# Performance work log

Measured on AMD Instinct MI355X. Metric: run time of the kernel, lower is better.

## Reference

```python
import jax, jax.numpy as jnp
import numpy as np

NEG_BIG = -9.0e15

def setup_inputs() -> dict:
    key = jax.random.key(0)
    k1, k2, k3, k4 = jax.random.split(key, 4)
    N, F_in, F_out = 2048, 512, 64
    x = jax.random.normal(k1, (N, F_in), dtype=jnp.float32)
    adj = jax.random.randint(k2, (N, N), 0, 2, dtype=jnp.int32)
    # xavier_uniform with gain=1.414
    def xavier(k, shape, gain=1.414):
        fan_in, fan_out = shape[0], shape[1]
        bound = gain * np.sqrt(6.0 / (fan_in + fan_out))
        return jax.random.uniform(k, shape, jnp.float32, -bound, bound)
    W = xavier(k3, (F_in, F_out))
    a = xavier(k4, (F_out, 1))
    return {"x": x, "adj": adj, "W": W, "a": a}

def reference(x, adj, W, a):
    h = x @ W                                  # [N, F_out]
    # pairwise |h_i - h_j| projected by a: e[i,j] = relu(sum_f |h_i,f - h_j,f| * a_f)
    diff = jnp.abs(h[:, None, :] - h[None, :, :])   # [N, N, F_out]
    e = jax.nn.relu(jnp.einsum('ijf,fo->ij', diff, a))  # [N, N]
    scores = jnp.where(adj > 0, e, NEG_BIG)
    attention = jax.nn.softmax(scores, axis=1)
    out = attention @ h                        # [N, F_out]
    return jax.nn.relu(out)                    # concat=True path
```

## Files before the change

kernel.cpp:

```cpp
#include <hip/hip_runtime.h>

#define Nn 2048
#define FIN 512
#define FO 64
#define SHIFT 20.0f
#define NJT 2
#define JSEG 1024
#define CHK 256

typedef __attribute__((ext_vector_type(8))) short bf16x8;
typedef __attribute__((ext_vector_type(4))) float f32x4;

__device__ __forceinline__ unsigned rne_bf16(float x) {
    unsigned u = __float_as_uint(x);
    return (u + 0x7FFFu + ((u >> 16) & 1u)) >> 16;
}
__device__ __forceinline__ float bf16_f32(unsigned s) { return __uint_as_float(s << 16); }

__global__ __launch_bounds__(256) void gat_xw(const float* __restrict__ x,
                                              const float* __restrict__ W,
                                              float* __restrict__ h) {
    __shared__ float part[2][2][FO];
    const int wave = threadIdx.x >> 6;
    const int lane = threadIdx.x & 63;
    const int rs = wave >> 1;
    const int kh = wave & 1;
    int row = blockIdx.x * 2 + rs;
    row = __builtin_amdgcn_readfirstlane(row);
    const float* xr = x + (size_t)row * FIN + kh * (FIN / 2);
    const float* Wp = W + (size_t)kh * (FIN / 2) * FO;
    float acc = 0.f;
#pragma unroll 2
    for (int k = 0; k < FIN / 2; k += 8) {
        float4 xa = *(const float4*)(xr + k);
        float4 xb = *(const float4*)(xr + k + 4);
        acc = fmaf(xa.x, Wp[(k + 0) * FO + lane], acc);
        acc = fmaf(xa.y, Wp[(k + 1) * FO + lane], acc);
        acc = fmaf(xa.z, Wp[(k + 2) * FO + lane], acc);
        acc = fmaf(xa.w, Wp[(k + 3) * FO + lane], acc);
        acc = fmaf(xb.x, Wp[(k + 4) * FO + lane], acc);
        acc = fmaf(xb.y, Wp[(k + 5) * FO + lane], acc);
        acc = fmaf(xb.z, Wp[(k + 6) * FO + lane], acc);
        acc = fmaf(xb.w, Wp[(k + 7) * FO + lane], acc);
    }
    part[rs][kh][lane] = acc;
    __syncthreads();
    if (threadIdx.x < 128) {
        const int r2 = threadIdx.x >> 6;
        const int l2 = threadIdx.x & 63;
        h[((size_t)blockIdx.x * 2 + r2) * FO + l2] = part[r2][0][l2] + part[r2][1][l2];
    }
}

__global__ __launch_bounds__(256) void gat_tr(const float* __restrict__ h,
                                              unsigned short* __restrict__ hbT_hi,
                                              unsigned short* __restrict__ hbT_lo) {
    __shared__ float t_s[64 * 68];
    const int tid = threadIdx.x;
    const int j0 = blockIdx.x * 64;
    for (int g4 = tid; g4 < 1024; g4 += 256) {
        float4 v = *(const float4*)(h + (size_t)j0 * FO + (size_t)g4 * 4);
        *(float4*)&t_s[(g4 >> 4) * 68 + (g4 & 15) * 4] = v;
    }
    __syncthreads();
    const int f = tid >> 2, q = tid & 3;
    unsigned* dh = (unsigned*)&hbT_hi[(size_t)f * Nn + j0 + q * 16];
    unsigned* dl = (unsigned*)&hbT_lo[(size_t)f * Nn + j0 + q * 16];
#pragma unroll
    for (int u = 0; u < 8; u++) {
        float x0 = t_s[(q * 16 + 2 * u) * 68 + f];
        float x1 = t_s[(q * 16 + 2 * u + 1) * 68 + f];
        unsigned h0 = rne_bf16(x0), h1 = rne_bf16(x1);
        dh[u] = h0 | (h1 << 16);
        float r0 = x0 - bf16_f32(h0), r1 = x1 - bf16_f32(h1);
        dl[u] = rne_bf16(r0) | (rne_bf16(r1) << 16);
    }
}

__global__ __launch_bounds__(256) void gat_attn7(const float* __restrict__ h,
                                                 const int* __restrict__ adj,
                                                 const float* __restrict__ a,
                                                 const unsigned short* __restrict__ hbT_hi,
                                                 const unsigned short* __restrict__ hbT_lo,
                                                 float* __restrict__ opart,
                                                 float* __restrict__ lpart) {
    __shared__ float hj_s[CHK * 64];
    __shared__ unsigned short Ph_s[16 * 264];
    __shared__ unsigned short Pl_s[16 * 264];

    const int tid = threadIdx.x;
    const int it = blockIdx.x >> 1;
    const int jt = blockIdx.x & 1;
    const int ib = it * 16;
    const int jb = jt * JSEG;
    const int ig = __builtin_amdgcn_readfirstlane(tid >> 7);
    const int jg = tid & 127;
    const int lane = tid & 63;
    const int w = tid >> 6;
    const int m = lane & 15;
    const int g = lane >> 4;

    float ls[8] = {0.f, 0.f, 0.f, 0.f, 0.f, 0.f, 0.f, 0.f};
    f32x4 acc = {0.f, 0.f, 0.f, 0.f};

    for (int jc = 0; jc < JSEG; jc += CHK) {
        __syncthreads();
        const float* hsrc = h + (size_t)(jb + jc) * FO;
        for (int g4 = tid; g4 < 4096; g4 += 256) {
            const int j = g4 >> 4, c = g4 & 15;
            *(float4*)&hj_s[j * 64 + ((c ^ (j & 7)) << 2)] =
                *(const float4*)(hsrc + (size_t)g4 * 4);
        }
        __syncthreads();

        const int j0 = jg * 2, j1 = j0 + 1;
        int2 am[8];
        const int* adjp = adj + (size_t)(ib + ig * 8) * Nn + (jb + jc + j0);
#pragma unroll
        for (int ii = 0; ii < 8; ii++) am[ii] = *(const int2*)(adjp + (size_t)ii * Nn);

        float e[8][2];
#pragma unroll
        for (int ii = 0; ii < 8; ii++) e[ii][0] = e[ii][1] = 0.f;

#pragma unroll 2
        for (int fq = 0; fq < 16; fq++) {
            const int f = fq * 4;
            const float4 av = *(const float4*)(a + f);
            const float4 hj0 = *(const float4*)&hj_s[j0 * 64 + ((fq ^ (j0 & 7)) << 2)];
            const float4 hj1 = *(const float4*)&hj_s[j1 * 64 + ((fq ^ (j1 & 7)) << 2)];
#pragma unroll
            for (int ii = 0; ii < 8; ii++) {
                const float4 hi = *(const float4*)(h + (size_t)(ib + ig * 8 + ii) * FO + f);
                e[ii][0] = fmaf(fabsf(hi.x - hj0.x), av.x, e[ii][0]);
                e[ii][0] = fmaf(fabsf(hi.y - hj0.y), av.y, e[ii][0]);
                e[ii][0] = fmaf(fabsf(hi.z - hj0.z), av.z, e[ii][0]);
                e[ii][0] = fmaf(fabsf(hi.w - hj0.w), av.w, e[ii][0]);
                e[ii][1] = fmaf(fabsf(hi.x - hj1.x), av.x, e[ii][1]);
                e[ii][1] = fmaf(fabsf(hi.y - hj1.y), av.y, e[ii][1]);
                e[ii][1] = fmaf(fabsf(hi.z - hj1.z), av.z, e[ii][1]);
                e[ii][1] = fmaf(fabsf(hi.w - hj1.w), av.w, e[ii][1]);
            }
        }

#pragma unroll
        for (int ii = 0; ii < 8; ii++) {
            const float p0 = (am[ii].x > 0) ? __expf(fmaxf(e[ii][0], 0.f) - SHIFT) : 0.f;
            const float p1 = (am[ii].y > 0) ? __expf(fmaxf(e[ii][1], 0.f) - SHIFT) : 0.f;
            ls[ii] += p0 + p1;
            const unsigned h0 = rne_bf16(p0), h1 = rne_bf16(p1);
            const float r0 = p0 - bf16_f32(h0), r1 = p1 - bf16_f32(h1);
            ((unsigned*)Ph_s)[(ig * 8 + ii) * 132 + jg] = h0 | (h1 << 16);
            ((unsigned*)Pl_s)[(ig * 8 + ii) * 132 + jg] =
                rne_bf16(r0) | (rne_bf16(r1) << 16);
        }
        __syncthreads();

        const size_t bbase = (size_t)(w * 16 + m) * Nn + (jb + jc);
#pragma unroll
        for (int ks = 0; ks < 8; ks++) {
            const bf16x8 af = *(const bf16x8*)&Ph_s[m * 264 + ks * 32 + g * 8];
            const bf16x8 al = *(const bf16x8*)&Pl_s[m * 264 + ks * 32 + g * 8];
            const bf16x8 bh = *(const bf16x8*)&hbT_hi[bbase + ks * 32 + g * 8];
            const bf16x8 bl = *(const bf16x8*)&hbT_lo[bbase + ks * 32 + g * 8];
            acc = __builtin_amdgcn_mfma_f32_16x16x32_bf16(af, bh, acc, 0, 0, 0);
            acc = __builtin_amdgcn_mfma_f32_16x16x32_bf16(af, bl, acc, 0, 0, 0);
            acc = __builtin_amdgcn_mfma_f32_16x16x32_bf16(al, bh, acc, 0, 0, 0);
        }
    }

    __syncthreads();
    float* red = hj_s;
#pragma unroll
    for (int ii = 0; ii < 8; ii++) red[(ig * 8 + ii) * 132 + jg] = ls[ii];
    __syncthreads();
    if (tid < 16) {
        float l = 0.f;
        for (int c2 = 0; c2 < 128; c2++) l += red[tid * 132 + c2];
        lpart[(size_t)jt * Nn + ib + tid] = l;
    }
#pragma unroll
    for (int r = 0; r < 4; r++)
        opart[((size_t)jt * Nn + ib + g * 4 + r) * FO + w * 16 + m] = acc[r];
}

__global__ __launch_bounds__(256) void gat_merge(const float* __restrict__ opart,
                                                 const float* __restrict__ lpart,
                                                 float* __restrict__ out) {
    const int t = blockIdx.x * 256 + threadIdx.x;
    const int i = t >> 6;
    const float o = opart[t] + opart[(size_t)Nn * FO + t];
    const float l = lpart[i] + lpart[Nn + i];
    out[t] = fmaxf(o / l, 0.f);
}

extern "C" void kernel_launch(void* const* d_in, const int* in_sizes, int n_in,
                              void* d_out, int out_size, void* d_ws, size_t ws_size,
                              hipStream_t stream) {
    const float* x   = (const float*)d_in[0];
    const int*   adj = (const int*)d_in[1];
    const float* W   = (const float*)d_in[2];
    const float* a   = (const float*)d_in[3];
    float* out = (float*)d_out;

    float* h     = (float*)d_ws;
    float* opart = h + (size_t)Nn * FO;
    float* lpart = opart + (size_t)NJT * Nn * FO;
    unsigned short* hbT_hi = (unsigned short*)(lpart + (size_t)NJT * Nn);
    unsigned short* hbT_lo = hbT_hi + (size_t)FO * Nn;

    gat_xw<<<dim3(1024), dim3(256), 0, stream>>>(x, W, h);
    gat_tr<<<dim3(32), dim3(256), 0, stream>>>(h, hbT_hi, hbT_lo);
    gat_attn7<<<dim3(256), dim3(256), 0, stream>>>(h, adj, a, hbT_hi, hbT_lo, opart, lpart);
    gat_merge<<<dim3(512), dim3(256), 0, stream>>>(opart, lpart, out);
}
```

Measured before the change: 140.3 us.

## Split attention over more j-segments chosen by workspace size, halve chunk size

The attention kernel now takes a runtime number of j-segments (2, 4 or 8, picked from the available workspace), launching up to 1024 blocks instead of 256 to fill more compute units. Each thread handles one j column instead of two, and the chunk size drops to 128 so shared memory shrinks and launch bounds request 3 blocks per unit. The shared h tile uses padding instead of an XOR swizzle. The merge kernel loops over the segments, which adds partial-result traffic and merge work for the extra parallelism.

Result: slower. 149.4 us (+6.5%).

```diff
diff --git a/kernel.cpp b/kernel.cpp
--- a/kernel.cpp
+++ b/kernel.cpp
@@ -4,9 +4,7 @@
 #define FIN 512
 #define FO 64
 #define SHIFT 20.0f
-#define NJT 2
-#define JSEG 1024
-#define CHK 256
+#define CHK 128
 
 typedef __attribute__((ext_vector_type(8))) short bf16x8;
 typedef __attribute__((ext_vector_type(4))) float f32x4;
@@ -77,22 +75,25 @@
     }
 }
 
-__global__ __launch_bounds__(256) void gat_attn7(const float* __restrict__ h,
-                                                 const int* __restrict__ adj,
-                                                 const float* __restrict__ a,
-                                                 const unsigned short* __restrict__ hbT_hi,
-                                                 const unsigned short* __restrict__ hbT_lo,
-                                                 float* __restrict__ opart,
-                                                 float* __restrict__ lpart) {
-    __shared__ float hj_s[CHK * 64];
-    __shared__ unsigned short Ph_s[16 * 264];
-    __shared__ unsigned short Pl_s[16 * 264];
+__global__ __launch_bounds__(256, 3) void gat_attn8(const float* __restrict__ h,
+                                                    const int* __restrict__ adj,
+                                                    const float* __restrict__ a,
+                                                    const unsigned short* __restrict__ hbT_hi,
+                                                    const unsigned short* __restrict__ hbT_lo,
+                                                    float* __restrict__ opart,
+                                                    float* __restrict__ lpart,
+                                                    int njt_log2) {
+    __shared__ float hj_s[CHK * 68];
+    __shared__ unsigned short Ph_s[16 * 136];
+    __shared__ unsigned short Pl_s[16 * 136];
 
     const int tid = threadIdx.x;
-    const int it = blockIdx.x >> 1;
-    const int jt = blockIdx.x & 1;
+    const int njt = 1 << njt_log2;
+    const int jseg = Nn >> njt_log2;
+    const int it = blockIdx.x >> njt_log2;
+    const int jt = blockIdx.x & (njt - 1);
     const int ib = it * 16;
-    const int jb = jt * JSEG;
+    const int jb = jt * jseg;
     const int ig = __builtin_amdgcn_readfirstlane(tid >> 7);
     const int jg = tid & 127;
     const int lane = tid & 63;
@@ -102,65 +103,59 @@
 
     float ls[8] = {0.f, 0.f, 0.f, 0.f, 0.f, 0.f, 0.f, 0.f};
     f32x4 acc = {0.f, 0.f, 0.f, 0.f};
-
-    for (int jc = 0; jc < JSEG; jc += CHK) {
+    const float* hi_base = h + (size_t)(ib + ig * 8) * FO;
+
+    for (int jc = 0; jc < jseg; jc += CHK) {
         __syncthreads();
         const float* hsrc = h + (size_t)(jb + jc) * FO;
-        for (int g4 = tid; g4 < 4096; g4 += 256) {
-            const int j = g4 >> 4, c = g4 & 15;
-            *(float4*)&hj_s[j * 64 + ((c ^ (j & 7)) << 2)] =
+#pragma unroll
+        for (int u = 0; u < 8; u++) {
+            const int g4 = u * 256 + tid;
+            *(float4*)&hj_s[(g4 >> 4) * 68 + (g4 & 15) * 4] =
                 *(const float4*)(hsrc + (size_t)g4 * 4);
         }
         __syncthreads();
 
-        const int j0 = jg * 2, j1 = j0 + 1;
-        int2 am[8];
-        const int* adjp = adj + (size_t)(ib + ig * 8) * Nn + (jb + jc + j0);
-#pragma unroll
-        for (int ii = 0; ii < 8; ii++) am[ii] = *(const int2*)(adjp + (size_t)ii * Nn);
-
-        float e[8][2];
-#pragma unroll
-        for (int ii = 0; ii < 8; ii++) e[ii][0] = e[ii][1] = 0.f;
-
-#pragma unroll 2
+        int amv[8];
+        const int* adjp = adj + (size_t)(ib + ig * 8) * Nn + (jb + jc + jg);
+#pragma unroll
+        for (int ii = 0; ii < 8; ii++) amv[ii] = adjp[(size_t)ii * Nn];
+
+        float e[8];
+#pragma unroll
+        for (int ii = 0; ii < 8; ii++) e[ii] = 0.f;
+
+#pragma unroll 4
         for (int fq = 0; fq < 16; fq++) {
             const int f = fq * 4;
+            const float4 hj = *(const float4*)&hj_s[jg * 68 + f];
             const float4 av = *(const float4*)(a + f);
-            const float4 hj0 = *(const float4*)&hj_s[j0 * 64 + ((fq ^ (j0 & 7)) << 2)];
-            const float4 hj1 = *(const float4*)&hj_s[j1 * 64 + ((fq ^ (j1 & 7)) << 2)];
 #pragma unroll
             for (int ii = 0; ii < 8; ii++) {
-                const float4 hi = *(const float4*)(h + (size_t)(ib + ig * 8 + ii) * FO + f);
-                e[ii][0] = fmaf(fabsf(hi.x - hj0.x), av.x, e[ii][0]);
-                e[ii][0] = fmaf(fabsf(hi.y - hj0.y), av.y, e[ii][0]);
-                e[ii][0] = fmaf(fabsf(hi.z - hj0.z), av.z, e[ii][0]);
-                e[ii][0] = fmaf(fabsf(hi.w - hj0.w), av.w, e[ii][0]);
-                e[ii][1] = fmaf(fabsf(hi.x - hj1.x), av.x, e[ii][1]);
-                e[ii][1] = fmaf(fabsf(hi.y - hj1.y), av.y, e[ii][1]);
-                e[ii][1] = fmaf(fabsf(hi.z - hj1.z), av.z, e[ii][1]);
-                e[ii][1] = fmaf(fabsf(hi.w - hj1.w), av.w, e[ii][1]);
+                const float4 hi = *(const float4*)(hi_base + ii * FO + f);
+                e[ii] = fmaf(fabsf(hi.x - hj.x), av.x, e[ii]);
+                e[ii] = fmaf(fabsf(hi.y - hj.y), av.y, e[ii]);
+                e[ii] = fmaf(fabsf(hi.z - hj.z), av.z, e[ii]);
+                e[ii] = fmaf(fabsf(hi.w - hj.w), av.w, e[ii]);
             }
         }
 
 #pragma unroll
         for (int ii = 0; ii < 8; ii++) {
-            const float p0 = (am[ii].x > 0) ? __expf(fmaxf(e[ii][0], 0.f) - SHIFT) : 0.f;
-            const float p1 = (am[ii].y > 0) ? __expf(fmaxf(e[ii][1], 0.f) - SHIFT) : 0.f;
-            ls[ii] += p0 + p1;
-            const unsigned h0 = rne_bf16(p0), h1 = rne_bf16(p1);
-            const float r0 = p0 - bf16_f32(h0), r1 = p1 - bf16_f32(h1);
-            ((unsigned*)Ph_s)[(ig * 8 + ii) * 132 + jg] = h0 | (h1 << 16);
-            ((unsigned*)Pl_s)[(ig * 8 + ii) * 132 + jg] =
-                rne_bf16(r0) | (rne_bf16(r1) << 16);
+            const float p = (amv[ii] > 0) ? __expf(fmaxf(e[ii], 0.f) - SHIFT) : 0.f;
+            ls[ii] += p;
+            const unsigned ph = rne_bf16(p);
+            const float r = p - bf16_f32(ph);
+            Ph_s[(ig * 8 + ii) * 136 + jg] = (unsigned short)ph;
+            Pl_s[(ig * 8 + ii) * 136 + jg] = (unsigned short)rne_bf16(r);
         }
         __syncthreads();
 
         const size_t bbase = (size_t)(w * 16 + m) * Nn + (jb + jc);
 #pragma unroll
-        for (int ks = 0; ks < 8; ks++) {
-            const bf16x8 af = *(const bf16x8*)&Ph_s[m * 264 + ks * 32 + g * 8];
-            const bf16x8 al = *(const bf16x8*)&Pl_s[m * 264 + ks * 32 + g * 8];
+        for (int ks = 0; ks < 4; ks++) {
+            const bf16x8 af = *(const bf16x8*)&Ph_s[m * 136 + ks * 32 + g * 8];
+            const bf16x8 al = *(const bf16x8*)&Pl_s[m * 136 + ks * 32 + g * 8];
             const bf16x8 bh = *(const bf16x8*)&hbT_hi[bbase + ks * 32 + g * 8];
             const bf16x8 bl = *(const bf16x8*)&hbT_lo[bbase + ks * 32 + g * 8];
             acc = __builtin_amdgcn_mfma_f32_16x16x32_bf16(af, bh, acc, 0, 0, 0);
@@ -186,11 +181,14 @@
 
 __global__ __launch_bounds__(256) void gat_merge(const float* __restrict__ opart,
                                                  const float* __restrict__ lpart,
-                                                 float* __restrict__ out) {
+                                                 float* __restrict__ out, int njt) {
     const int t = blockIdx.x * 256 + threadIdx.x;
     const int i = t >> 6;
-    const float o = opart[t] + opart[(size_t)Nn * FO + t];
-    const float l = lpart[i] + lpart[Nn + i];
+    float o = 0.f, l = 0.f;
+    for (int s = 0; s < njt; s++) {
+        o += opart[(size_t)s * Nn * FO + t];
+        l += lpart[(size_t)s * Nn + i];
+    }
     out[t] = fmaxf(o / l, 0.f);
 }
 
@@ -203,14 +201,20 @@
     const float* a   = (const float*)d_in[3];
     float* out = (float*)d_out;
 
+    int njt_log2 = 1;
+    if (ws_size >= (size_t)1048576 + 8u * 532480u + 65536u) njt_log2 = 3;
+    else if (ws_size >= (size_t)1048576 + 4u * 532480u + 65536u) njt_log2 = 2;
+    const int njt = 1 << njt_log2;
+
     float* h     = (float*)d_ws;
     float* opart = h + (size_t)Nn * FO;
-    float* lpart = opart + (size_t)NJT * Nn * FO;
-    unsigned short* hbT_hi = (unsigned short*)(lpart + (size_t)NJT * Nn);
+    float* lpart = opart + (size_t)njt * Nn * FO;
+    unsigned short* hbT_hi = (unsigned short*)(lpart + (size_t)njt * Nn);
     unsigned short* hbT_lo = hbT_hi + (size_t)FO * Nn;
 
     gat_xw<<<dim3(1024), dim3(256), 0, stream>>>(x, W, h);
     gat_tr<<<dim3(32), dim3(256), 0, stream>>>(h, hbT_hi, hbT_lo);
-    gat_attn7<<<dim3(256), dim3(256), 0, stream>>>(h, adj, a, hbT_hi, hbT_lo, opart, lpart);
-    gat_merge<<<dim3(512), dim3(256), 0, stream>>>(opart, lpart, out);
-}
+    gat_attn8<<<dim3(128 * njt), dim3(256), 0, stream>>>(h, adj, a, hbT_hi, hbT_lo,
+                                                         opart, lpart, njt_log2);
+    gat_merge<<<dim3(512), dim3(256), 0, stream>>>(opart, lpart, out, njt);
+}
```
